# Optimization experiments

Hardware: AMD Instinct MI355X
Metric: run time of the kernel (lower is better)

## Reference

```python
import jax, jax.numpy as jnp
import numpy as np

EPS = 1e-6
BN_EPS = 1e-5


def _grid_idx(loc, Hg, Wg):
    # loc: [B, N0, 2] in [-1, 1], (x, y) order -> nearest cell index in Hg x Wg grid
    loc = jnp.clip(loc, -1.0, 1.0)
    px = jnp.clip(jnp.round(0.5 * (loc[..., 0] + 1.0) * Wg - 0.5).astype(jnp.int32), 0, Wg - 1)
    py = jnp.clip(jnp.round(0.5 * (loc[..., 1] + 1.0) * Hg - 0.5).astype(jnp.int32), 0, Hg - 1)
    return py * Wg + px  # [B, N0]


def token2map(x, loc_orig, idx_agg, H, W):
    # scatter-average token features into an H x W map via the original points
    B, N, C = x.shape
    idx_hw = _grid_idx(loc_orig, H, W)                         # [B, N0]
    feat = jnp.take_along_axis(x, idx_agg[..., None], axis=1)  # [B, N0, C]
    ssum = jax.vmap(lambda s, i, f: s.at[i].add(f))(jnp.zeros((B, H * W, C), x.dtype), idx_hw, feat)
    cnt = jax.vmap(lambda c, i: c.at[i].add(1.0))(jnp.zeros((B, H * W), x.dtype), idx_hw)
    return (ssum / (cnt[..., None] + EPS)).reshape(B, H, W, C)


def map2token(x_map, N, loc_orig, idx_agg, agg_weight):
    # bilinear gather from map at original points, then weighted scatter-mean to N tokens
    B, Hd, Wd, C = x_map.shape
    loc = jnp.clip(loc_orig, -1.0, 1.0)
    fx = jnp.clip(0.5 * (loc[..., 0] + 1.0) * Wd - 0.5, 0.0, Wd - 1.0)
    fy = jnp.clip(0.5 * (loc[..., 1] + 1.0) * Hd - 0.5, 0.0, Hd - 1.0)
    x0 = jnp.floor(fx); y0 = jnp.floor(fy)
    wx = fx - x0; wy = fy - y0
    x0i = x0.astype(jnp.int32); y0i = y0.astype(jnp.int32)
    x1i = jnp.minimum(x0i + 1, Wd - 1); y1i = jnp.minimum(y0i + 1, Hd - 1)
    mp = x_map.reshape(B, Hd * Wd, C)
    g = lambda iy, ix: jnp.take_along_axis(mp, (iy * Wd + ix)[..., None], axis=1)  # [B, N0, C]
    f = (((1 - wx) * (1 - wy))[..., None] * g(y0i, x0i)
         + (wx * (1 - wy))[..., None] * g(y0i, x1i)
         + ((1 - wx) * wy)[..., None] * g(y1i, x0i)
         + (wx * wy)[..., None] * g(y1i, x1i))
    wpt = agg_weight[..., 0]                                   # [B, N0]
    num = jax.vmap(lambda n, i, s: n.at[i].add(s))(jnp.zeros((B, N, C), f.dtype), idx_agg, f * wpt[..., None])
    den = jax.vmap(lambda d, i, w: d.at[i].add(w))(jnp.zeros((B, N), f.dtype), idx_agg, wpt)
    return num / (den[..., None] + EPS)


def token_cluster_grid(x, loc_orig, idx_agg, agg_weight, weight, Hc, Wc):
    # weighted merge of tokens into Hc x Wc coarse grid cells (keyed by original points)
    B, N, C = x.shape
    Ns = Hc * Wc
    idx_cell = _grid_idx(loc_orig, Hc, Wc)                     # [B, N0] -> new token id
    wtok = weight[..., 0]                                      # [B, N] token confidence weight
    wpt = jnp.take_along_axis(wtok, idx_agg, axis=1)           # [B, N0]
    fpt = jnp.take_along_axis(x, idx_agg[..., None], axis=1)   # [B, N0, C]
    num = jax.vmap(lambda n, i, s: n.at[i].add(s))(jnp.zeros((B, Ns, C), x.dtype), idx_cell, fpt * wpt[..., None])
    den = jax.vmap(lambda d, i, w: d.at[i].add(w))(jnp.zeros((B, Ns), x.dtype), idx_cell, wpt)
    x_down = num / (den[..., None] + EPS)
    weight_t = (wpt / (jnp.take_along_axis(den, idx_cell, axis=1) + EPS))[..., None]  # [B, N0, 1]
    agg_weight_down = agg_weight * weight_t
    agg_weight_down = agg_weight_down / jnp.max(agg_weight_down, axis=1, keepdims=True)
    return x_down, idx_cell, agg_weight_down


def setup_inputs() -> dict:
    key = jax.random.key(0)
    ks = jax.random.split(key, 8)
    B, N, C_in, C_out = 4, 16384, 128, 256
    H = W = 256
    N0 = H * W
    x = jax.random.normal(ks[0], (B, N, C_in), jnp.float32)
    loc_orig = jax.random.uniform(ks[1], (B, N0, 2), jnp.float32, -1.0, 1.0)
    idx_agg = jax.random.randint(ks[2], (B, N0), 0, N, jnp.int32)
    agg_weight = jax.random.uniform(ks[3], (B, N0, 1), jnp.float32)
    conv_w = jax.random.normal(ks[4], (3, 3, C_in, C_out), jnp.float32) / np.sqrt(9 * C_in).astype(np.float32)
    conv_b = jnp.zeros((C_out,), jnp.float32)
    skip_w = jax.random.normal(ks[5], (C_out, C_in), jnp.float32) / np.sqrt(C_in).astype(np.float32)
    bn_gamma = jnp.ones((C_out,), jnp.float32)
    bn_beta = jnp.zeros((C_out,), jnp.float32)
    conf_w = jax.random.normal(ks[6], (1, C_out), jnp.float32) / np.sqrt(C_out).astype(np.float32)
    conf_b = jnp.zeros((1,), jnp.float32)
    return {"x": x, "loc_orig": loc_orig, "idx_agg": idx_agg, "agg_weight": agg_weight,
            "conv_w": conv_w, "conv_b": conv_b, "skip_w": skip_w,
            "bn_gamma": bn_gamma, "bn_beta": bn_beta, "conf_w": conf_w, "conf_b": conf_b,
            "H": H, "W": W}


def reference(x, loc_orig, idx_agg, agg_weight, conv_w, conv_b, skip_w, bn_gamma, bn_beta, conf_w, conf_b, H, W):
    B, N, C = x.shape
    # scatter tokens to map, 3x3 s2 conv
    x_map = token2map(x, loc_orig, idx_agg, H, W)              # [B, H, W, C]
    y = jax.lax.conv_general_dilated(x_map, conv_w, (2, 2), ((1, 1), (1, 1)),
                                     dimension_numbers=("NHWC", "HWIO", "NHWC")) + conv_b
    Hd = (H - 1) // 2 + 1
    Wd = (W - 1) // 2 + 1
    # gather back to tokens + linear skip
    tok = map2token(y, N, loc_orig, idx_agg, agg_weight) + x @ skip_w.T   # [B, N, C_out]
    # BatchNorm2d over tokens (train-mode batch stats, per channel)
    mu = jnp.mean(tok, axis=(0, 1))
    var = jnp.var(tok, axis=(0, 1))
    tokn = (tok - mu) / jnp.sqrt(var + BN_EPS) * bn_gamma + bn_beta
    conf = tokn @ conf_w.T + conf_b                            # [B, N, 1]
    weight = jnp.exp(conf)
    # grid clustering: merge to (Hd//2) x (Wd//2) cells = N * sample_ratio tokens
    x_down, idx_agg_down, agg_weight_down = token_cluster_grid(tokn, loc_orig, idx_agg, agg_weight, weight, Hd // 2, Wd // 2)
    x_down = jax.nn.relu(x_down)
    x_out = jax.nn.relu(tokn)
    return x_down, x_out, conf, agg_weight_down, idx_agg_down
```

## Files before the change

### kernel.cpp

```cpp
#include <hip/hip_runtime.h>
#include <hip/hip_bf16.h>
#include <math.h>

#define BB    4
#define NTOK  16384
#define CIN   128
#define COUT  256
#define HM    256
#define WM    256
#define NP    65536
#define HD    128
#define WD    128
#define HC    64
#define WC    64
#define NS    4096
#define EPS   1e-6f
#define BNEPS 1e-5f

#define SEG_TOK  (BB * NP)
#define SEG_64   (SEG_TOK + BB * NTOK)
#define NSEG     (SEG_64 + BB * NS)

typedef __attribute__((ext_vector_type(8))) short bfrag8;
typedef __attribute__((ext_vector_type(4))) float ffrag4;

static constexpr size_t BNSUM_OFF  = 0;
static constexpr size_t BNSQ_OFF   = BNSUM_OFF + 256;
static constexpr size_t MAXW_OFF   = BNSQ_OFF + 256;
static constexpr size_t CNTS_OFF   = MAXW_OFF + 256;
static constexpr size_t CURS_OFF   = CNTS_OFF + NSEG;
static constexpr size_t ZERO_FLOATS = CURS_OFF + NSEG;
static constexpr size_t YBUF_OFF   = (ZERO_FLOATS + 255) & ~(size_t)255;
static constexpr size_t XMAPN_OFF  = YBUF_OFF + (size_t)BB * HD * WD * COUT / 2;
static constexpr size_t XBF_OFF    = XMAPN_OFF + (size_t)BB * NP * CIN / 2;
static constexpr size_t TOKB_OFF   = XBF_OFF + (size_t)BB * NTOK * CIN / 2;
static constexpr size_t WFRAG_OFF  = TOKB_OFF + (size_t)BB * NTOK * COUT / 2;
static constexpr size_t SFRAG_OFF  = WFRAG_OFF + (size_t)9 * 4 * 16 * 512 / 2;
static constexpr size_t WEXP_OFF   = SFRAG_OFF + (size_t)4 * 16 * 512 / 2;
static constexpr size_t AWDT_OFF   = WEXP_OFF + (size_t)BB * NTOK;
static constexpr size_t ABUF_OFF   = AWDT_OFF + (size_t)BB * NP;
static constexpr size_t BBUF_OFF   = ABUF_OFF + 256;
static constexpr size_t CWA_OFF    = BBUF_OFF + 256;
static constexpr size_t C0_OFF     = CWA_OFF + 256;
static constexpr size_t CELL256_OFF = C0_OFF + 256;
static constexpr size_t CELL64_OFF  = CELL256_OFF + (size_t)BB * NP;
static constexpr size_t DEN1_OFF   = CELL64_OFF + (size_t)BB * NP;
static constexpr size_t DEN2_OFF   = DEN1_OFF + (size_t)BB * NTOK;
static constexpr size_t STARTS_OFF = DEN2_OFF + (size_t)BB * NS;
static constexpr size_t BLKSUM_OFF = STARTS_OFF + NSEG;
static constexpr size_t BLKEXCL_OFF = BLKSUM_OFF + 512;
static constexpr size_t PIDX_OFF   = BLKEXCL_OFF + 512;


__device__ __forceinline__ unsigned short f2bf(float f) {
    unsigned int u = __float_as_uint(f);
    return (unsigned short)((u + 0x7FFFu + ((u >> 16) & 1u)) >> 16);
}
__device__ __forceinline__ float bf2f(unsigned short u) {
    return __uint_as_float((unsigned int)u << 16);
}


__global__ void k_cells(const float* __restrict__ loc, int* __restrict__ cell256,
                        int* __restrict__ cell64) {
    int i = blockIdx.x * 256 + threadIdx.x;
    float lx = fminf(fmaxf(loc[2 * (size_t)i], -1.f), 1.f);
    float ly = fminf(fmaxf(loc[2 * (size_t)i + 1], -1.f), 1.f);
    int px = (int)rintf(0.5f * (lx + 1.f) * WM - 0.5f);
    px = min(max(px, 0), WM - 1);
    int py = (int)rintf(0.5f * (ly + 1.f) * HM - 0.5f);
    py = min(max(py, 0), HM - 1);
    cell256[i] = py * WM + px;
    int qx = (int)rintf(0.5f * (lx + 1.f) * WC - 0.5f);
    qx = min(max(qx, 0), WC - 1);
    int qy = (int)rintf(0.5f * (ly + 1.f) * HC - 0.5f);
    qy = min(max(qy, 0), HC - 1);
    cell64[i] = qy * WC + qx;
}

__global__ void k_xcast(const float* __restrict__ x, unsigned short* __restrict__ xbf) {
    size_t i = (size_t)blockIdx.x * 256 + threadIdx.x;
    float4 v = ((const float4*)x)[i];
    ushort4 o;
    o.x = f2bf(v.x); o.y = f2bf(v.y); o.z = f2bf(v.z); o.w = f2bf(v.w);
    ((ushort4*)xbf)[i] = o;
}

__global__ void k_hist(const int* __restrict__ cell256, const int* __restrict__ idx_agg,
                       const int* __restrict__ cell64, int* __restrict__ cnts) {
    int gp = blockIdx.x * 256 + threadIdx.x;
    int b = gp >> 16;
    atomicAdd(&cnts[b * NP + cell256[gp]], 1);
    atomicAdd(&cnts[SEG_TOK + b * NTOK + idx_agg[gp]], 1);
    atomicAdd(&cnts[SEG_64 + b * NS + cell64[gp]], 1);
}

__global__ __launch_bounds__(256) void k_scan1(const int* __restrict__ cnts,
                                               int* __restrict__ starts,
                                               int* __restrict__ blksum) {
    int t = threadIdx.x;
    int base = blockIdx.x * 1024 + t * 4;
    int4 v = *(const int4*)(cnts + base);
    int tsum = v.x + v.y + v.z + v.w;
    __shared__ int s[256];
    s[t] = tsum;
    __syncthreads();
    for (int off = 1; off < 256; off <<= 1) {
        int add = (t >= off) ? s[t - off] : 0;
        __syncthreads();
        s[t] += add;
        __syncthreads();
    }
    int excl = s[t] - tsum;
    int4 o;
    o.x = excl; o.y = excl + v.x; o.z = o.y + v.y; o.w = o.z + v.z;
    *(int4*)(starts + base) = o;
    if (t == 255) blksum[blockIdx.x] = s[255];
}

__global__ __launch_bounds__(512) void k_scan2(const int* __restrict__ blksum,
                                               int* __restrict__ blkexcl) {
    int t = threadIdx.x;
    __shared__ int s[512];
    int v = (t < 336) ? blksum[t] : 0;
    s[t] = v;
    __syncthreads();
    for (int off = 1; off < 512; off <<= 1) {
        int add = (t >= off) ? s[t - off] : 0;
        __syncthreads();
        s[t] += add;
        __syncthreads();
    }
    if (t < 336) blkexcl[t] = s[t] - v;
}

__global__ void k_fill(const int* __restrict__ cell256, const int* __restrict__ idx_agg,
                       const int* __restrict__ cell64, const int* __restrict__ starts,
                       const int* __restrict__ blkexcl, int* __restrict__ curs,
                       int* __restrict__ pidx) {
    int gp = blockIdx.x * 256 + threadIdx.x;
    int b = gp >> 16;
    int ia = idx_agg[gp];
    int t1 = b * NP + cell256[gp];
    int p1 = starts[t1] + blkexcl[t1 >> 10] + atomicAdd(&curs[t1], 1);
    pidx[p1] = ia;
    int t2 = SEG_TOK + b * NTOK + ia;
    int p2 = starts[t2] + blkexcl[t2 >> 10] + atomicAdd(&curs[t2], 1);
    pidx[p2] = gp;
    int t3 = SEG_64 + b * NS + cell64[gp];
    int p3 = starts[t3] + blkexcl[t3 >> 10] + atomicAdd(&curs[t3], 1);
    pidx[p3] = ia;
}

__global__ __launch_bounds__(256) void k_gather_map(const unsigned short* __restrict__ xbf,
                                                    const int* __restrict__ starts,
                                                    const int* __restrict__ blkexcl,
                                                    const int* __restrict__ cnts,
                                                    const int* __restrict__ pidx,
                                                    unsigned short* __restrict__ xmapn) {
    int tgt = blockIdx.x * 8 + (threadIdx.x >> 5);
    int lane = threadIdx.x & 31;
    int b = tgt >> 16;
    int start = starts[tgt] + blkexcl[tgt >> 10];
    int cnt = cnts[tgt];
    float4 acc = make_float4(0.f, 0.f, 0.f, 0.f);
    for (int j = 0; j < cnt; ++j) {
        int tk = pidx[start + j];
        ushort4 u = *(const ushort4*)(xbf + ((size_t)b * NTOK + tk) * CIN + lane * 4);
        acc.x += bf2f(u.x); acc.y += bf2f(u.y); acc.z += bf2f(u.z); acc.w += bf2f(u.w);
    }
    float inv = 1.0f / ((float)cnt + EPS);
    ushort4 o;
    o.x = f2bf(acc.x * inv);
    o.y = f2bf(acc.y * inv);
    o.z = f2bf(acc.z * inv);
    o.w = f2bf(acc.w * inv);
    *(ushort4*)(xmapn + (size_t)tgt * CIN + lane * 4) = o;
}

__global__ void k_wfrag(const float* __restrict__ cw, unsigned short* __restrict__ wfrag) {
    int i = blockIdx.x * 256 + threadIdx.x;
    int j = i & 7;
    int lane = (i >> 3) & 63;
    int nt = (i >> 9) & 15;
    int kc = (i >> 13) & 3;
    int khw = i >> 15;
    int c = kc * 32 + ((lane >> 4) << 3) + j;
    int n = nt * 16 + (lane & 15);
    wfrag[i] = f2bf(cw[((size_t)khw * CIN + c) * COUT + n]);
}

__global__ void k_sfrag(const float* __restrict__ sw, unsigned short* __restrict__ sfrag) {
    int i = blockIdx.x * 256 + threadIdx.x;
    int j = i & 7;
    int lane = (i >> 3) & 63;
    int nt = (i >> 9) & 15;
    int kc = i >> 13;
    int c = kc * 32 + ((lane >> 4) << 3) + j;
    int n = nt * 16 + (lane & 15);
    sfrag[i] = f2bf(sw[(size_t)n * CIN + c]);
}

__global__ __launch_bounds__(256) void k_convmf(const unsigned short* __restrict__ xmapn,
                                                const unsigned short* __restrict__ wfrag,
                                                const float* __restrict__ cb,
                                                unsigned short* __restrict__ y) {
    int bz = blockIdx.x;
    int ow0 = (bz & 1) * 64;
    int oh = (bz >> 1) & (HD - 1);
    int b = bz >> 8;
    int tid = threadIdx.x;
    int w = tid >> 6, lane = tid & 63;
    int n0 = w * 64;

    __shared__ unsigned short s_even[65 * 136];
    __shared__ unsigned short s_odd[64 * 136];

    ffrag4 acc[4][4];
#pragma unroll
    for (int mt = 0; mt < 4; ++mt)
#pragma unroll
        for (int nt = 0; nt < 4; ++nt) {
            ffrag4 z = {0.f, 0.f, 0.f, 0.f};
            acc[mt][nt] = z;
        }

    int iw0 = 2 * ow0 - 1;
    int lm = lane & 15;
    int lq = lane >> 4;
    int cbase = lq << 3;

    for (int kh = 0; kh < 3; ++kh) {
        int ih = 2 * oh - 1 + kh;
        __syncthreads();
        {
            const unsigned short* rowb =
                xmapn + ((size_t)b * NP + (size_t)ih * WM) * CIN;
            bool ihok = (ih >= 0 && ih < HM);
            for (int idx = tid; idx < 129 * 16; idx += 256) {
                int pix = idx >> 4;
                int c8 = (idx & 15) * 8;
                int iw = iw0 + pix;
                uint4 v = make_uint4(0u, 0u, 0u, 0u);
                if (ihok && iw >= 0 && iw < WM)
                    v = *(const uint4*)(rowb + (size_t)iw * CIN + c8);
                unsigned short* dst = (pix & 1)
                    ? &s_odd[(size_t)((pix - 1) >> 1) * 136 + c8]
                    : &s_even[(size_t)(pix >> 1) * 136 + c8];
                *(uint4*)dst = v;
            }
        }
        __syncthreads();
#pragma unroll
        for (int kw = 0; kw < 3; ++kw) {
            int khw = kh * 3 + kw;
#pragma unroll
            for (int kc = 0; kc < 4; ++kc) {
                int c = kc * 32 + cbase;
                bfrag8 af[4];
#pragma unroll
                for (int mt = 0; mt < 4; ++mt) {
                    int m = mt * 16 + lm;
                    const unsigned short* src;
                    if (kw == 1)      src = &s_odd[(size_t)m * 136 + c];
                    else if (kw == 0) src = &s_even[(size_t)m * 136 + c];
                    else              src = &s_even[(size_t)(m + 1) * 136 + c];
                    af[mt] = *(const bfrag8*)(const void*)src;
                }
                const unsigned short* wb =
                    wfrag + ((size_t)((khw * 4 + kc) * 16) + w * 4) * 512 + lane * 8;
#pragma unroll
                for (int nt = 0; nt < 4; ++nt) {
                    bfrag8 bf = *(const bfrag8*)(const void*)(wb + (size_t)nt * 512);
#pragma unroll
                    for (int mt = 0; mt < 4; ++mt)
                        acc[mt][nt] = __builtin_amdgcn_mfma_f32_16x16x32_bf16(
                            af[mt], bf, acc[mt][nt], 0, 0, 0);
                }
            }
        }
    }

    unsigned short* yb = y + (((size_t)b * HD + oh) * WD + ow0) * COUT;
#pragma unroll
    for (int nt = 0; nt < 4; ++nt) {
        int n = n0 + nt * 16 + lm;
        float bias = cb[n];
#pragma unroll
        for (int mt = 0; mt < 4; ++mt) {
#pragma unroll
            for (int r = 0; r < 4; ++r) {
                int m = mt * 16 + lq * 4 + r;
                yb[(size_t)m * COUT + n] = f2bf(acc[mt][nt][r] + bias);
            }
        }
    }
}

__global__ __launch_bounds__(256) void k_gather_tok(const unsigned short* __restrict__ y,
                                                    const float* __restrict__ loc,
                                                    const float* __restrict__ aggw,
                                                    const int* __restrict__ starts,
                                                    const int* __restrict__ blkexcl,
                                                    const int* __restrict__ cnts,
                                                    const int* __restrict__ pidx,
                                                    float* __restrict__ num_out,
                                                    float* __restrict__ den1) {
    int wv = threadIdx.x >> 6, lane = threadIdx.x & 63;
    int tl = blockIdx.x * 4 + wv;
    int b = tl >> 14;
    int tgt = SEG_TOK + tl;
    int start = starts[tgt] + blkexcl[tgt >> 10];
    int cnt = cnts[tgt];
    const unsigned short* ybase = y + (size_t)b * (HD * WD * COUT);
    float4 num = make_float4(0.f, 0.f, 0.f, 0.f);
    float den = 0.f;
    for (int j = 0; j < cnt; ++j) {
        int gp = pidx[start + j];
        float lx = fminf(fmaxf(loc[2 * (size_t)gp], -1.f), 1.f);
        float ly = fminf(fmaxf(loc[2 * (size_t)gp + 1], -1.f), 1.f);
        float fx = fminf(fmaxf(0.5f * (lx + 1.f) * WD - 0.5f, 0.f), (float)(WD - 1));
        float fy = fminf(fmaxf(0.5f * (ly + 1.f) * HD - 0.5f, 0.f), (float)(HD - 1));
        float x0f = floorf(fx), y0f = floorf(fy);
        float wx = fx - x0f, wy = fy - y0f;
        int x0 = (int)x0f, y0 = (int)y0f;
        int x1 = min(x0 + 1, WD - 1), y1 = min(y0 + 1, HD - 1);
        ushort4 u00 = *(const ushort4*)(ybase + ((size_t)y0 * WD + x0) * COUT + lane * 4);
        ushort4 u01 = *(const ushort4*)(ybase + ((size_t)y0 * WD + x1) * COUT + lane * 4);
        ushort4 u10 = *(const ushort4*)(ybase + ((size_t)y1 * WD + x0) * COUT + lane * 4);
        ushort4 u11 = *(const ushort4*)(ybase + ((size_t)y1 * WD + x1) * COUT + lane * 4);
        float w00 = (1.f - wx) * (1.f - wy), w01 = wx * (1.f - wy);
        float w10 = (1.f - wx) * wy, w11 = wx * wy;
        float aw = aggw[gp];
        num.x += (w00 * bf2f(u00.x) + w01 * bf2f(u01.x) + w10 * bf2f(u10.x) + w11 * bf2f(u11.x)) * aw;
        num.y += (w00 * bf2f(u00.y) + w01 * bf2f(u01.y) + w10 * bf2f(u10.y) + w11 * bf2f(u11.y)) * aw;
        num.z += (w00 * bf2f(u00.z) + w01 * bf2f(u01.z) + w10 * bf2f(u10.z) + w11 * bf2f(u11.z)) * aw;
        num.w += (w00 * bf2f(u00.w) + w01 * bf2f(u01.w) + w10 * bf2f(u10.w) + w11 * bf2f(u11.w)) * aw;
        den += aw;
    }
    *(float4*)(num_out + (size_t)tl * COUT + lane * 4) = num;
    if (lane == 0) den1[tl] = den;
}

__global__ __launch_bounds__(256) void k_tokmf(const unsigned short* __restrict__ xbf,
                                               const unsigned short* __restrict__ sfrag,
                                               const float* __restrict__ den1,
                                               float* __restrict__ tok) {
    int t0 = blockIdx.x * 64;
    int tid = threadIdx.x;
    int w = tid >> 6, lane = tid & 63;
    int n0 = w * 64;
    int lm = lane & 15, lq = lane >> 4;

    __shared__ unsigned short s_x[64 * 136];
    const unsigned short* xb = xbf + (size_t)t0 * CIN;
    for (int idx = tid; idx < 64 * 16; idx += 256) {
        int row = idx >> 4, c8 = (idx & 15) * 8;
        *(uint4*)&s_x[(size_t)row * 136 + c8] = *(const uint4*)(xb + (size_t)row * CIN + c8);
    }
    __syncthreads();

    ffrag4 acc[4][4];
#pragma unroll
    for (int mt = 0; mt < 4; ++mt)
#pragma unroll
        for (int nt = 0; nt < 4; ++nt) {
            ffrag4 z = {0.f, 0.f, 0.f, 0.f};
            acc[mt][nt] = z;
        }

#pragma unroll
    for (int kc = 0; kc < 4; ++kc) {
        int c = kc * 32 + lq * 8;
        bfrag8 af[4];
#pragma unroll
        for (int mt = 0; mt < 4; ++mt)
            af[mt] = *(const bfrag8*)(const void*)&s_x[(size_t)(mt * 16 + lm) * 136 + c];
        const unsigned short* sb = sfrag + ((size_t)(kc * 16) + w * 4) * 512 + lane * 8;
#pragma unroll
        for (int nt = 0; nt < 4; ++nt) {
            bfrag8 bf = *(const bfrag8*)(const void*)(sb + (size_t)nt * 512);
#pragma unroll
            for (int mt = 0; mt < 4; ++mt)
                acc[mt][nt] = __builtin_amdgcn_mfma_f32_16x16x32_bf16(
                    af[mt], bf, acc[mt][nt], 0, 0, 0);
        }
    }

#pragma unroll
    for (int mt = 0; mt < 4; ++mt) {
#pragma unroll
        for (int r = 0; r < 4; ++r) {
            int tkn = t0 + mt * 16 + lq * 4 + r;
            float inv = 1.f / (den1[tkn] + EPS);
#pragma unroll
            for (int nt = 0; nt < 4; ++nt) {
                int n = n0 + nt * 16 + lm;
                size_t a = (size_t)tkn * COUT + n;
                tok[a] = tok[a] * inv + acc[mt][nt][r];
            }
        }
    }
}

__global__ void k_bnstats(const float* __restrict__ tok, float* __restrict__ bnsum,
                          float* __restrict__ bnsq) {
    int k = threadIdx.x;
    size_t t0 = (size_t)blockIdx.x * 256;
    float s = 0.f, sq = 0.f;
    for (int t = 0; t < 256; ++t) {
        float v = tok[(t0 + t) * COUT + k];
        s += v;
        sq = fmaf(v, v, sq);
    }
    atomicAdd(bnsum + k, s);
    atomicAdd(bnsq + k, sq);
}

__global__ void k_bnparams(const float* __restrict__ bnsum, const float* __restrict__ bnsq,
                           const float* __restrict__ gamma, const float* __restrict__ beta,
                           const float* __restrict__ confw, const float* __restrict__ confb,
                           float* __restrict__ abuf, float* __restrict__ bbuf,
                           float* __restrict__ cwa, float* __restrict__ c0) {
    int k = threadIdx.x;
    const float cntv = (float)(BB * NTOK);
    float mu = bnsum[k] / cntv;
    float var = bnsq[k] / cntv - mu * mu;
    float a = gamma[k] * rsqrtf(var + BNEPS);
    float bbv = beta[k] - mu * a;
    abuf[k] = a;
    bbuf[k] = bbv;
    float cw = confw[k];
    cwa[k] = a * cw;
    __shared__ float red[256];
    red[k] = bbv * cw;
    __syncthreads();
    for (int s = 128; s > 0; s >>= 1) {
        if (k < s) red[k] += red[k + s];
        __syncthreads();
    }
    if (k == 0) c0[0] = red[0] + confb[0];
}

__global__ void k_conf(const float* __restrict__ tok, const float* __restrict__ cwa,
                       const float* __restrict__ c0v, const float* __restrict__ abuf,
                       const float* __restrict__ bbuf, float* __restrict__ conf_out,
                       unsigned short* __restrict__ tokb, float* __restrict__ wexp) {
    int tid = threadIdx.x;
    int tkn = blockIdx.x * 16 + (tid >> 4);
    int kc = (tid & 15) * 16;
    const float* row = tok + (size_t)tkn * COUT + kc;
    unsigned short* tb = tokb + (size_t)tkn * COUT + kc;
    float s = 0.f;
#pragma unroll
    for (int i = 0; i < 16; i += 4) {
        float4 v = *(const float4*)(row + i);
        float4 w = *(const float4*)(cwa + kc + i);
        float4 a = *(const float4*)(abuf + kc + i);
        float4 bb = *(const float4*)(bbuf + kc + i);
        s += v.x * w.x + v.y * w.y + v.z * w.z + v.w * w.w;
        ushort4 o;
        o.x = f2bf(fmaf(a.x, v.x, bb.x));
        o.y = f2bf(fmaf(a.y, v.y, bb.y));
        o.z = f2bf(fmaf(a.z, v.z, bb.z));
        o.w = f2bf(fmaf(a.w, v.w, bb.w));
        *(ushort4*)(tb + i) = o;
    }
    for (int off = 8; off > 0; off >>= 1) s += __shfl_down(s, off, 16);
    if ((tid & 15) == 0) {
        float cv = s + c0v[0];
        conf_out[tkn] = cv;
        wexp[tkn] = expf(cv);
    }
}

__global__ __launch_bounds__(256) void k_gather_cluster(const unsigned short* __restrict__ tokb,
                                                        const float* __restrict__ wexp,
                                                        const int* __restrict__ starts,
                                                        const int* __restrict__ blkexcl,
                                                        const int* __restrict__ cnts,
                                                        const int* __restrict__ pidx,
                                                        float* __restrict__ xdown,
                                                        float* __restrict__ den2) {
    int wv = threadIdx.x >> 6, lane = threadIdx.x & 63;
    int tl = blockIdx.x * 4 + wv;
    int b = tl >> 12;
    int tgt = SEG_64 + tl;
    int start = starts[tgt] + blkexcl[tgt >> 10];
    int cnt = cnts[tgt];
    float4 num = make_float4(0.f, 0.f, 0.f, 0.f);
    float den = 0.f;
    for (int j = 0; j < cnt; ++j) {
        int ia = pidx[start + j];
        float w = wexp[(size_t)b * NTOK + ia];
        ushort4 u = *(const ushort4*)(tokb + ((size_t)b * NTOK + ia) * COUT + lane * 4);
        num.x = fmaf(bf2f(u.x), w, num.x);
        num.y = fmaf(bf2f(u.y), w, num.y);
        num.z = fmaf(bf2f(u.z), w, num.z);
        num.w = fmaf(bf2f(u.w), w, num.w);
        den += w;
    }
    float inv = 1.f / (den + EPS);
    float4 o;
    o.x = fmaxf(num.x * inv, 0.f);
    o.y = fmaxf(num.y * inv, 0.f);
    o.z = fmaxf(num.z * inv, 0.f);
    o.w = fmaxf(num.w * inv, 0.f);
    *(float4*)(xdown + (size_t)tl * COUT + lane * 4) = o;
    if (lane == 0) den2[tl] = den;
}

__global__ void k_awd1(const float* __restrict__ wexp, const float* __restrict__ den2,
                       const int* __restrict__ idx_agg, const int* __restrict__ cell64,
                       const float* __restrict__ aggw, float* __restrict__ awdt,
                       float* __restrict__ idx_out_f, unsigned int* __restrict__ maxw) {
    int b = blockIdx.x >> 6;
    int chunk = blockIdx.x & 63;
    int base = b * NP + chunk * 1024;
    float lmax = 0.f;
    for (int t = threadIdx.x; t < 1024; t += 256) {
        int gp = base + t;
        int ia = idx_agg[gp];
        int cell = cell64[gp];
        float w = wexp[(size_t)b * NTOK + ia];
        float wt = w / (den2[(size_t)b * NS + cell] + EPS);
        float tv = aggw[gp] * wt;
        awdt[gp] = tv;
        idx_out_f[gp] = (float)cell;
        lmax = fmaxf(lmax, tv);
    }
    __shared__ float red[256];
    red[threadIdx.x] = lmax;
    __syncthreads();
    for (int s = 128; s > 0; s >>= 1) {
        if (threadIdx.x < s) red[threadIdx.x] = fmaxf(red[threadIdx.x], red[threadIdx.x + s]);
        __syncthreads();
    }
    if (threadIdx.x == 0) atomicMax(maxw + b, __float_as_uint(red[0]));
}

__global__ void k_awd2(const float* __restrict__ awdt, const unsigned int* __restrict__ maxw,
                       float* __restrict__ awd_out) {
    int i = blockIdx.x * 256 + threadIdx.x;
    int b = i >> 16;
    awd_out[i] = awdt[i] / __uint_as_float(maxw[b]);
}

__global__ void k_relutok(float* __restrict__ tok, const float* __restrict__ abuf,
                          const float* __restrict__ bbuf) {
    size_t i = (size_t)blockIdx.x * 256 + threadIdx.x;
    int k4 = (int)(i & 63) * 4;
    float4 a = *(const float4*)(abuf + k4);
    float4 bb = *(const float4*)(bbuf + k4);
    float4 v = ((float4*)tok)[i];
    v.x = fmaxf(fmaf(a.x, v.x, bb.x), 0.f);
    v.y = fmaxf(fmaf(a.y, v.y, bb.y), 0.f);
    v.z = fmaxf(fmaf(a.z, v.z, bb.z), 0.f);
    v.w = fmaxf(fmaf(a.w, v.w, bb.w), 0.f);
    ((float4*)tok)[i] = v;
}

extern "C" void kernel_launch(void* const* d_in, const int* in_sizes, int n_in,
                              void* d_out, int out_size, void* d_ws, size_t ws_size,
                              hipStream_t stream) {
    const float* x        = (const float*)d_in[0];
    const float* loc      = (const float*)d_in[1];
    const int*   idx_agg  = (const int*)d_in[2];
    const float* aggw     = (const float*)d_in[3];
    const float* conv_w   = (const float*)d_in[4];
    const float* conv_b   = (const float*)d_in[5];
    const float* skip_w   = (const float*)d_in[6];
    const float* bn_gamma = (const float*)d_in[7];
    const float* bn_beta  = (const float*)d_in[8];
    const float* conf_w   = (const float*)d_in[9];
    const float* conf_b   = (const float*)d_in[10];

    float* ws      = (float*)d_ws;
    float* bnsum   = ws + BNSUM_OFF;
    float* bnsq    = ws + BNSQ_OFF;
    unsigned int* maxw = (unsigned int*)(ws + MAXW_OFF);
    int*   cnts    = (int*)(ws + CNTS_OFF);
    int*   curs    = (int*)(ws + CURS_OFF);
    unsigned short* ybuf  = (unsigned short*)(ws + YBUF_OFF);
    unsigned short* xmapn = (unsigned short*)(ws + XMAPN_OFF);
    unsigned short* xbf   = (unsigned short*)(ws + XBF_OFF);
    unsigned short* tokb  = (unsigned short*)(ws + TOKB_OFF);
    unsigned short* wfrag = (unsigned short*)(ws + WFRAG_OFF);
    unsigned short* sfrag = (unsigned short*)(ws + SFRAG_OFF);
    float* wexp    = ws + WEXP_OFF;
    float* awdt    = ws + AWDT_OFF;
    float* abuf    = ws + ABUF_OFF;
    float* bbuf    = ws + BBUF_OFF;
    float* cwa     = ws + CWA_OFF;
    float* c0      = ws + C0_OFF;
    int*   cell256 = (int*)(ws + CELL256_OFF);
    int*   cell64  = (int*)(ws + CELL64_OFF);
    float* den1    = ws + DEN1_OFF;
    float* den2    = ws + DEN2_OFF;
    int*   starts  = (int*)(ws + STARTS_OFF);
    int*   blksum  = (int*)(ws + BLKSUM_OFF);
    int*   blkexcl = (int*)(ws + BLKEXCL_OFF);
    int*   pidx    = (int*)(ws + PIDX_OFF);

    float* out       = (float*)d_out;
    float* out_xdown = out;
    float* out_x     = out + (size_t)BB * NS * COUT;
    float* out_conf  = out_x + (size_t)BB * NTOK * COUT;
    float* out_awd   = out_conf + (size_t)BB * NTOK;
    float* out_idx   = out_awd + (size_t)BB * NP;

    hipMemsetAsync(d_ws, 0, ZERO_FLOATS * sizeof(float), stream);

    k_cells<<<BB * NP / 256, 256, 0, stream>>>(loc, cell256, cell64);
    k_xcast<<<BB * NTOK * CIN / 4 / 256, 256, 0, stream>>>(x, xbf);
    k_wfrag<<<9 * 4 * 16 * 512 / 256, 256, 0, stream>>>(conv_w, wfrag);
    k_sfrag<<<4 * 16 * 512 / 256, 256, 0, stream>>>(skip_w, sfrag);
    k_hist<<<BB * NP / 256, 256, 0, stream>>>(cell256, idx_agg, cell64, cnts);
    k_scan1<<<NSEG / 1024, 256, 0, stream>>>(cnts, starts, blksum);
    k_scan2<<<1, 512, 0, stream>>>(blksum, blkexcl);
    k_fill<<<BB * NP / 256, 256, 0, stream>>>(cell256, idx_agg, cell64, starts,
                                              blkexcl, curs, pidx);
    k_gather_map<<<BB * NP / 8, 256, 0, stream>>>(xbf, starts, blkexcl, cnts, pidx, xmapn);
    k_convmf<<<BB * HD * 2, 256, 0, stream>>>(xmapn, wfrag, conv_b, ybuf);
    k_gather_tok<<<BB * NTOK / 4, 256, 0, stream>>>(ybuf, loc, aggw, starts, blkexcl,
                                                    cnts, pidx, out_x, den1);
    k_tokmf<<<BB * NTOK / 64, 256, 0, stream>>>(xbf, sfrag, den1, out_x);
    k_bnstats<<<BB * NTOK / 256, 256, 0, stream>>>(out_x, bnsum, bnsq);
    k_bnparams<<<1, 256, 0, stream>>>(bnsum, bnsq, bn_gamma, bn_beta, conf_w, conf_b,
                                      abuf, bbuf, cwa, c0);
    k_conf<<<BB * NTOK / 16, 256, 0, stream>>>(out_x, cwa, c0, abuf, bbuf,
                                               out_conf, tokb, wexp);
    k_gather_cluster<<<BB * NS / 4, 256, 0, stream>>>(tokb, wexp, starts, blkexcl,
                                                      cnts, pidx, out_xdown, den2);
    k_awd1<<<BB * 64, 256, 0, stream>>>(wexp, den2, idx_agg, cell64, aggw,
                                        awdt, out_idx, maxw);
    k_awd2<<<BB * NP / 256, 256, 0, stream>>>(awdt, maxw, out_awd);
    k_relutok<<<BB * NTOK * COUT / 4 / 256, 256, 0, stream>>>(out_x, abuf, bbuf);
}
```

Before: 535.9 us.

## Fuse token gather, skip GEMM, BN stats, and relu into fewer kernels

Merges cell computation with the histogram, folds the bilinear token gather into the skip-GEMM kernel with the normalized gather result staged in shared memory as bf16, accumulates BatchNorm sums in the GEMM epilogue, and writes the relu output inside the conf kernel. This removes several full passes over the fp32 token tensor and multiple launches. In exchange, each block now gathers 64 tokens serially per wave before its MFMA work, which lowers parallelism in the gather phase. The gather term is also rounded to bf16 before the add, which changes precision.

```diff
diff --git a/kernel.cpp b/kernel.cpp
--- a/kernel.cpp
+++ b/kernel.cpp
@@ -44,8 +44,7 @@
 static constexpr size_t C0_OFF     = CWA_OFF + 256;
 static constexpr size_t CELL256_OFF = C0_OFF + 256;
 static constexpr size_t CELL64_OFF  = CELL256_OFF + (size_t)BB * NP;
-static constexpr size_t DEN1_OFF   = CELL64_OFF + (size_t)BB * NP;
-static constexpr size_t DEN2_OFF   = DEN1_OFF + (size_t)BB * NTOK;
+static constexpr size_t DEN2_OFF   = CELL64_OFF + (size_t)BB * NP;
 static constexpr size_t STARTS_OFF = DEN2_OFF + (size_t)BB * NS;
 static constexpr size_t BLKSUM_OFF = STARTS_OFF + NSEG;
 static constexpr size_t BLKEXCL_OFF = BLKSUM_OFF + 512;
@@ -61,21 +60,28 @@
 }
 
 
-__global__ void k_cells(const float* __restrict__ loc, int* __restrict__ cell256,
-                        int* __restrict__ cell64) {
+__global__ void k_cellhist(const float* __restrict__ loc, const int* __restrict__ idx_agg,
+                           int* __restrict__ cell256, int* __restrict__ cell64,
+                           int* __restrict__ cnts) {
     int i = blockIdx.x * 256 + threadIdx.x;
+    int b = i >> 16;
     float lx = fminf(fmaxf(loc[2 * (size_t)i], -1.f), 1.f);
     float ly = fminf(fmaxf(loc[2 * (size_t)i + 1], -1.f), 1.f);
     int px = (int)rintf(0.5f * (lx + 1.f) * WM - 0.5f);
     px = min(max(px, 0), WM - 1);
     int py = (int)rintf(0.5f * (ly + 1.f) * HM - 0.5f);
     py = min(max(py, 0), HM - 1);
-    cell256[i] = py * WM + px;
+    int c256 = py * WM + px;
+    cell256[i] = c256;
     int qx = (int)rintf(0.5f * (lx + 1.f) * WC - 0.5f);
     qx = min(max(qx, 0), WC - 1);
     int qy = (int)rintf(0.5f * (ly + 1.f) * HC - 0.5f);
     qy = min(max(qy, 0), HC - 1);
-    cell64[i] = qy * WC + qx;
+    int c64 = qy * WC + qx;
+    cell64[i] = c64;
+    atomicAdd(&cnts[b * NP + c256], 1);
+    atomicAdd(&cnts[SEG_TOK + b * NTOK + idx_agg[i]], 1);
+    atomicAdd(&cnts[SEG_64 + b * NS + c64], 1);
 }
 
 __global__ void k_xcast(const float* __restrict__ x, unsigned short* __restrict__ xbf) {
@@ -84,15 +90,6 @@
     ushort4 o;
     o.x = f2bf(v.x); o.y = f2bf(v.y); o.z = f2bf(v.z); o.w = f2bf(v.w);
     ((ushort4*)xbf)[i] = o;
-}
-
-__global__ void k_hist(const int* __restrict__ cell256, const int* __restrict__ idx_agg,
-                       const int* __restrict__ cell64, int* __restrict__ cnts) {
-    int gp = blockIdx.x * 256 + threadIdx.x;
-    int b = gp >> 16;
-    atomicAdd(&cnts[b * NP + cell256[gp]], 1);
-    atomicAdd(&cnts[SEG_TOK + b * NTOK + idx_agg[gp]], 1);
-    atomicAdd(&cnts[SEG_64 + b * NS + cell64[gp]], 1);
 }
 
 __global__ __launch_bounds__(256) void k_scan1(const int* __restrict__ cnts,
@@ -297,69 +294,68 @@
     }
 }
 
-__global__ __launch_bounds__(256) void k_gather_tok(const unsigned short* __restrict__ y,
-                                                    const float* __restrict__ loc,
-                                                    const float* __restrict__ aggw,
-                                                    const int* __restrict__ starts,
-                                                    const int* __restrict__ blkexcl,
-                                                    const int* __restrict__ cnts,
-                                                    const int* __restrict__ pidx,
-                                                    float* __restrict__ num_out,
-                                                    float* __restrict__ den1) {
-    int wv = threadIdx.x >> 6, lane = threadIdx.x & 63;
-    int tl = blockIdx.x * 4 + wv;
-    int b = tl >> 14;
-    int tgt = SEG_TOK + tl;
-    int start = starts[tgt] + blkexcl[tgt >> 10];
-    int cnt = cnts[tgt];
-    const unsigned short* ybase = y + (size_t)b * (HD * WD * COUT);
-    float4 num = make_float4(0.f, 0.f, 0.f, 0.f);
-    float den = 0.f;
-    for (int j = 0; j < cnt; ++j) {
-        int gp = pidx[start + j];
-        float lx = fminf(fmaxf(loc[2 * (size_t)gp], -1.f), 1.f);
-        float ly = fminf(fmaxf(loc[2 * (size_t)gp + 1], -1.f), 1.f);
-        float fx = fminf(fmaxf(0.5f * (lx + 1.f) * WD - 0.5f, 0.f), (float)(WD - 1));
-        float fy = fminf(fmaxf(0.5f * (ly + 1.f) * HD - 0.5f, 0.f), (float)(HD - 1));
-        float x0f = floorf(fx), y0f = floorf(fy);
-        float wx = fx - x0f, wy = fy - y0f;
-        int x0 = (int)x0f, y0 = (int)y0f;
-        int x1 = min(x0 + 1, WD - 1), y1 = min(y0 + 1, HD - 1);
-        ushort4 u00 = *(const ushort4*)(ybase + ((size_t)y0 * WD + x0) * COUT + lane * 4);
-        ushort4 u01 = *(const ushort4*)(ybase + ((size_t)y0 * WD + x1) * COUT + lane * 4);
-        ushort4 u10 = *(const ushort4*)(ybase + ((size_t)y1 * WD + x0) * COUT + lane * 4);
-        ushort4 u11 = *(const ushort4*)(ybase + ((size_t)y1 * WD + x1) * COUT + lane * 4);
-        float w00 = (1.f - wx) * (1.f - wy), w01 = wx * (1.f - wy);
-        float w10 = (1.f - wx) * wy, w11 = wx * wy;
-        float aw = aggw[gp];
-        num.x += (w00 * bf2f(u00.x) + w01 * bf2f(u01.x) + w10 * bf2f(u10.x) + w11 * bf2f(u11.x)) * aw;
-        num.y += (w00 * bf2f(u00.y) + w01 * bf2f(u01.y) + w10 * bf2f(u10.y) + w11 * bf2f(u11.y)) * aw;
-        num.z += (w00 * bf2f(u00.z) + w01 * bf2f(u01.z) + w10 * bf2f(u10.z) + w11 * bf2f(u11.z)) * aw;
-        num.w += (w00 * bf2f(u00.w) + w01 * bf2f(u01.w) + w10 * bf2f(u10.w) + w11 * bf2f(u11.w)) * aw;
-        den += aw;
-    }
-    *(float4*)(num_out + (size_t)tl * COUT + lane * 4) = num;
-    if (lane == 0) den1[tl] = den;
-}
-
-__global__ __launch_bounds__(256) void k_tokmf(const unsigned short* __restrict__ xbf,
-                                               const unsigned short* __restrict__ sfrag,
-                                               const float* __restrict__ den1,
-                                               float* __restrict__ tok) {
+__global__ __launch_bounds__(256) void k_gtokmf(const unsigned short* __restrict__ y,
+                                                const float* __restrict__ loc,
+                                                const float* __restrict__ aggw,
+                                                const unsigned short* __restrict__ xbf,
+                                                const unsigned short* __restrict__ sfrag,
+                                                const int* __restrict__ starts,
+                                                const int* __restrict__ blkexcl,
+                                                const int* __restrict__ cnts,
+                                                const int* __restrict__ pidx,
+                                                float* __restrict__ tok,
+                                                float* __restrict__ bnsum,
+                                                float* __restrict__ bnsq) {
     int t0 = blockIdx.x * 64;
     int tid = threadIdx.x;
     int w = tid >> 6, lane = tid & 63;
+    __shared__ unsigned short s_num[64 * 264];
+
+    for (int i = 0; i < 16; ++i) {
+        int row = w * 16 + i;
+        int tl = t0 + row;
+        int b = tl >> 14;
+        int tgt = SEG_TOK + tl;
+        int start = starts[tgt] + blkexcl[tgt >> 10];
+        int cnt = cnts[tgt];
+        const unsigned short* ybase = y + (size_t)b * (HD * WD * COUT);
+        float4 num = make_float4(0.f, 0.f, 0.f, 0.f);
+        float den = 0.f;
+        for (int j = 0; j < cnt; ++j) {
+            int gp = pidx[start + j];
+            float lx = fminf(fmaxf(loc[2 * (size_t)gp], -1.f), 1.f);
+            float ly = fminf(fmaxf(loc[2 * (size_t)gp + 1], -1.f), 1.f);
+            float fx = fminf(fmaxf(0.5f * (lx + 1.f) * WD - 0.5f, 0.f), (float)(WD - 1));
+            float fy = fminf(fmaxf(0.5f * (ly + 1.f) * HD - 0.5f, 0.f), (float)(HD - 1));
+            float x0f = floorf(fx), y0f = floorf(fy);
+            float wx = fx - x0f, wy = fy - y0f;
+            int x0 = (int)x0f, y0 = (int)y0f;
+            int x1 = min(x0 + 1, WD - 1), y1 = min(y0 + 1, HD - 1);
+            ushort4 u00 = *(const ushort4*)(ybase + ((size_t)y0 * WD + x0) * COUT + lane * 4);
+            ushort4 u01 = *(const ushort4*)(ybase + ((size_t)y0 * WD + x1) * COUT + lane * 4);
+            ushort4 u10 = *(const ushort4*)(ybase + ((size_t)y1 * WD + x0) * COUT + lane * 4);
+            ushort4 u11 = *(const ushort4*)(ybase + ((size_t)y1 * WD + x1) * COUT + lane * 4);
+            float w00 = (1.f - wx) * (1.f - wy), w01 = wx * (1.f - wy);
+            float w10 = (1.f - wx) * wy, w11 = wx * wy;
+            float aw = aggw[gp];
+            num.x += (w00 * bf2f(u00.x) + w01 * bf2f(u01.x) + w10 * bf2f(u10.x) + w11 * bf2f(u11.x)) * aw;
+            num.y += (w00 * bf2f(u00.y) + w01 * bf2f(u01.y) + w10 * bf2f(u10.y) + w11 * bf2f(u11.y)) * aw;
+            num.z += (w00 * bf2f(u00.z) + w01 * bf2f(u01.z) + w10 * bf2f(u10.z) + w11 * bf2f(u11.z)) * aw;
+            num.w += (w00 * bf2f(u00.w) + w01 * bf2f(u01.w) + w10 * bf2f(u10.w) + w11 * bf2f(u11.w)) * aw;
+            den += aw;
+        }
+        float inv = 1.f / (den + EPS);
+        ushort4 o;
+        o.x = f2bf(num.x * inv);
+        o.y = f2bf(num.y * inv);
+        o.z = f2bf(num.z * inv);
+        o.w = f2bf(num.w * inv);
+        *(ushort4*)&s_num[(size_t)row * 264 + lane * 4] = o;
+    }
+    __syncthreads();
+
+    int lm = lane & 15, lq = lane >> 4;
     int n0 = w * 64;
-    int lm = lane & 15, lq = lane >> 4;
-
-    __shared__ unsigned short s_x[64 * 136];
-    const unsigned short* xb = xbf + (size_t)t0 * CIN;
-    for (int idx = tid; idx < 64 * 16; idx += 256) {
-        int row = idx >> 4, c8 = (idx & 15) * 8;
-        *(uint4*)&s_x[(size_t)row * 136 + c8] = *(const uint4*)(xb + (size_t)row * CIN + c8);
-    }
-    __syncthreads();
-
     ffrag4 acc[4][4];
 #pragma unroll
     for (int mt = 0; mt < 4; ++mt)
@@ -368,14 +364,13 @@
             ffrag4 z = {0.f, 0.f, 0.f, 0.f};
             acc[mt][nt] = z;
         }
-
 #pragma unroll
     for (int kc = 0; kc < 4; ++kc) {
-        int c = kc * 32 + lq * 8;
         bfrag8 af[4];
 #pragma unroll
         for (int mt = 0; mt < 4; ++mt)
-            af[mt] = *(const bfrag8*)(const void*)&s_x[(size_t)(mt * 16 + lm) * 136 + c];
+            af[mt] = *(const bfrag8*)(const void*)(xbf +
+                     (size_t)(t0 + mt * 16 + lm) * CIN + kc * 32 + lq * 8);
         const unsigned short* sb = sfrag + ((size_t)(kc * 16) + w * 4) * 512 + lane * 8;
 #pragma unroll
         for (int nt = 0; nt < 4; ++nt) {
@@ -387,34 +382,39 @@
         }
     }
 
+    float bsum[4] = {0.f, 0.f, 0.f, 0.f};
+    float bsq[4] = {0.f, 0.f, 0.f, 0.f};
 #pragma unroll
     for (int mt = 0; mt < 4; ++mt) {
 #pragma unroll
         for (int r = 0; r < 4; ++r) {
-            int tkn = t0 + mt * 16 + lq * 4 + r;
-            float inv = 1.f / (den1[tkn] + EPS);
+            int row = mt * 16 + lq * 4 + r;
+            int tkn = t0 + row;
 #pragma unroll
             for (int nt = 0; nt < 4; ++nt) {
                 int n = n0 + nt * 16 + lm;
-                size_t a = (size_t)tkn * COUT + n;
-                tok[a] = tok[a] * inv + acc[mt][nt][r];
+                float v = bf2f(s_num[(size_t)row * 264 + n]) + acc[mt][nt][r];
+                tok[(size_t)tkn * COUT + n] = v;
+                bsum[nt] += v;
+                bsq[nt] = fmaf(v, v, bsq[nt]);
             }
         }
     }
-}
-
-__global__ void k_bnstats(const float* __restrict__ tok, float* __restrict__ bnsum,
-                          float* __restrict__ bnsq) {
-    int k = threadIdx.x;
-    size_t t0 = (size_t)blockIdx.x * 256;
-    float s = 0.f, sq = 0.f;
-    for (int t = 0; t < 256; ++t) {
-        float v = tok[(t0 + t) * COUT + k];
-        s += v;
-        sq = fmaf(v, v, sq);
-    }
-    atomicAdd(bnsum + k, s);
-    atomicAdd(bnsq + k, sq);
+#pragma unroll
+    for (int nt = 0; nt < 4; ++nt) {
+        bsum[nt] += __shfl_down(bsum[nt], 32);
+        bsq[nt] += __shfl_down(bsq[nt], 32);
+        bsum[nt] += __shfl_down(bsum[nt], 16);
+        bsq[nt] += __shfl_down(bsq[nt], 16);
+    }
+    if (lq == 0) {
+#pragma unroll
+        for (int nt = 0; nt < 4; ++nt) {
+            int n = n0 + nt * 16 + lm;
+            atomicAdd(&bnsum[n], bsum[nt]);
+            atomicAdd(&bnsq[n], bsq[nt]);
+        }
+    }
 }
 
 __global__ void k_bnparams(const float* __restrict__ bnsum, const float* __restrict__ bnsq,
@@ -442,14 +442,14 @@
     if (k == 0) c0[0] = red[0] + confb[0];
 }
 
-__global__ void k_conf(const float* __restrict__ tok, const float* __restrict__ cwa,
-                       const float* __restrict__ c0v, const float* __restrict__ abuf,
-                       const float* __restrict__ bbuf, float* __restrict__ conf_out,
-                       unsigned short* __restrict__ tokb, float* __restrict__ wexp) {
+__global__ void k_confrelu(float* __restrict__ tok, const float* __restrict__ cwa,
+                           const float* __restrict__ c0v, const float* __restrict__ abuf,
+                           const float* __restrict__ bbuf, float* __restrict__ conf_out,
+                           unsigned short* __restrict__ tokb, float* __restrict__ wexp) {
     int tid = threadIdx.x;
     int tkn = blockIdx.x * 16 + (tid >> 4);
     int kc = (tid & 15) * 16;
-    const float* row = tok + (size_t)tkn * COUT + kc;
+    float* row = tok + (size_t)tkn * COUT + kc;
     unsigned short* tb = tokb + (size_t)tkn * COUT + kc;
     float s = 0.f;
 #pragma unroll
@@ -459,12 +459,18 @@
         float4 a = *(const float4*)(abuf + kc + i);
         float4 bb = *(const float4*)(bbuf + kc + i);
         s += v.x * w.x + v.y * w.y + v.z * w.z + v.w * w.w;
+        float4 tn;
+        tn.x = fmaf(a.x, v.x, bb.x);
+        tn.y = fmaf(a.y, v.y, bb.y);
+        tn.z = fmaf(a.z, v.z, bb.z);
+        tn.w = fmaf(a.w, v.w, bb.w);
         ushort4 o;
-        o.x = f2bf(fmaf(a.x, v.x, bb.x));
-        o.y = f2bf(fmaf(a.y, v.y, bb.y));
-        o.z = f2bf(fmaf(a.z, v.z, bb.z));
-        o.w = f2bf(fmaf(a.w, v.w, bb.w));
+        o.x = f2bf(tn.x); o.y = f2bf(tn.y); o.z = f2bf(tn.z); o.w = f2bf(tn.w);
         *(ushort4*)(tb + i) = o;
+        float4 rl;
+        rl.x = fmaxf(tn.x, 0.f); rl.y = fmaxf(tn.y, 0.f);
+        rl.z = fmaxf(tn.z, 0.f); rl.w = fmaxf(tn.w, 0.f);
+        *(float4*)(row + i) = rl;
     }
     for (int off = 8; off > 0; off >>= 1) s += __shfl_down(s, off, 16);
     if ((tid & 15) == 0) {
@@ -546,20 +552,6 @@
     awd_out[i] = awdt[i] / __uint_as_float(maxw[b]);
 }
 
-__global__ void k_relutok(float* __restrict__ tok, const float* __restrict__ abuf,
-                          const float* __restrict__ bbuf) {
-    size_t i = (size_t)blockIdx.x * 256 + threadIdx.x;
-    int k4 = (int)(i & 63) * 4;
-    float4 a = *(const float4*)(abuf + k4);
-    float4 bb = *(const float4*)(bbuf + k4);
-    float4 v = ((float4*)tok)[i];
-    v.x = fmaxf(fmaf(a.x, v.x, bb.x), 0.f);
-    v.y = fmaxf(fmaf(a.y, v.y, bb.y), 0.f);
-    v.z = fmaxf(fmaf(a.z, v.z, bb.z), 0.f);
-    v.w = fmaxf(fmaf(a.w, v.w, bb.w), 0.f);
-    ((float4*)tok)[i] = v;
-}
-
 extern "C" void kernel_launch(void* const* d_in, const int* in_sizes, int n_in,
                               void* d_out, int out_size, void* d_ws, size_t ws_size,
                               hipStream_t stream) {
@@ -595,7 +587,6 @@
     float* c0      = ws + C0_OFF;
     int*   cell256 = (int*)(ws + CELL256_OFF);
     int*   cell64  = (int*)(ws + CELL64_OFF);
-    float* den1    = ws + DEN1_OFF;
     float* den2    = ws + DEN2_OFF;
     int*   starts  = (int*)(ws + STARTS_OFF);
     int*   blksum  = (int*)(ws + BLKSUM_OFF);
@@ -611,29 +602,26 @@
 
     hipMemsetAsync(d_ws, 0, ZERO_FLOATS * sizeof(float), stream);
 
-    k_cells<<<BB * NP / 256, 256, 0, stream>>>(loc, cell256, cell64);
     k_xcast<<<BB * NTOK * CIN / 4 / 256, 256, 0, stream>>>(x, xbf);
     k_wfrag<<<9 * 4 * 16 * 512 / 256, 256, 0, stream>>>(conv_w, wfrag);
     k_sfrag<<<4 * 16 * 512 / 256, 256, 0, stream>>>(skip_w, sfrag);
-    k_hist<<<BB * NP / 256, 256, 0, stream>>>(cell256, idx_agg, cell64, cnts);
+    k_cellhist<<<BB * NP / 256, 256, 0, stream>>>(loc, idx_agg, cell256, cell64, cnts);
     k_scan1<<<NSEG / 1024, 256, 0, stream>>>(cnts, starts, blksum);
     k_scan2<<<1, 512, 0, stream>>>(blksum, blkexcl);
     k_fill<<<BB * NP / 256, 256, 0, stream>>>(cell256, idx_agg, cell64, starts,
                                               blkexcl, curs, pidx);
     k_gather_map<<<BB * NP / 8, 256, 0, stream>>>(xbf, starts, blkexcl, cnts, pidx, xmapn);
     k_convmf<<<BB * HD * 2, 256, 0, stream>>>(xmapn, wfrag, conv_b, ybuf);
-    k_gather_tok<<<BB * NTOK / 4, 256, 0, stream>>>(ybuf, loc, aggw, starts, blkexcl,
-                                                    cnts, pidx, out_x, den1);
-    k_tokmf<<<BB * NTOK / 64, 256, 0, stream>>>(xbf, sfrag, den1, out_x);
-    k_bnstats<<<BB * NTOK / 256, 256, 0, stream>>>(out_x, bnsum, bnsq);
+    k_gtokmf<<<BB * NTOK / 64, 256, 0, stream>>>(ybuf, loc, aggw, xbf, sfrag,
+                                                 starts, blkexcl, cnts, pidx,
+                                                 out_x, bnsum, bnsq);
     k_bnparams<<<1, 256, 0, stream>>>(bnsum, bnsq, bn_gamma, bn_beta, conf_w, conf_b,
                                       abuf, bbuf, cwa, c0);
-    k_conf<<<BB * NTOK / 16, 256, 0, stream>>>(out_x, cwa, c0, abuf, bbuf,
-                                               out_conf, tokb, wexp);
+    k_confrelu<<<BB * NTOK / 16, 256, 0, stream>>>(out_x, cwa, c0, abuf, bbuf,
+                                                   out_conf, tokb, wexp);
     k_gather_cluster<<<BB * NS / 4, 256, 0, stream>>>(tokb, wexp, starts, blkexcl,
                                                       cnts, pidx, out_xdown, den2);
     k_awd1<<<BB * 64, 256, 0, stream>>>(wexp, den2, idx_agg, cell64, aggw,
                                         awdt, out_idx, maxw);
     k_awd2<<<BB * NP / 256, 256, 0, stream>>>(awdt, maxw, out_awd);
-    k_relutok<<<BB * NTOK * COUT / 4 / 256, 256, 0, stream>>>(out_x, abuf, bbuf);
-}
+}
```

Result: slower. 592.9 us (+10.6%).
